# Optimization experiments

Hardware: AMD Instinct MI355X
Metric: run time of the kernel (lower is better)

Reference implementation:

```python
import jax, jax.numpy as jnp
import numpy as np

M, K, N, G = 4096, 4096, 4096, 128


def setup_inputs() -> dict:
    key = jax.random.key(0)
    k1, k2, k3 = jax.random.split(key, 3)
    a = jax.random.normal(k1, (M, K), dtype=jnp.float16)
    # 4-bit unsigned quantized weights, values in [0, 16)
    w_q = jax.random.randint(k2, (K, N), 0, 16, dtype=jnp.int32)
    # group-wise scales: one per (k-group, n); small magnitude keeps fp16 output in range
    scale = jax.random.uniform(k3, (K // G, N), dtype=jnp.float16, minval=0.001, maxval=0.02)
    return {"a": a, "w_q": w_q, "scale": scale, "group_size": G}


def reference(a, w_q, scale, group_size):
    # Dequantize: w[k, n] = w_q[k, n] * scale[k // group_size, n]
    scale_full = jnp.repeat(scale, group_size, axis=0)  # [K, N]
    w = w_q.astype(a.dtype) * scale_full                # fp16 dequantized weight
    out = jnp.matmul(a, w, preferred_element_type=jnp.float32)
    return out.astype(jnp.float16)
```

## Files before the change

### kernel.cpp

```cpp
#include <hip/hip_runtime.h>
#include <hip/hip_fp16.h>

#define MDIM 4096
#define NDIM 4096
#define KDIM 4096

#define BM 128
#define BN 128
#define BK 64
#define NT 256

typedef _Float16 f16x8 __attribute__((ext_vector_type(8)));
typedef float f32x4 __attribute__((ext_vector_type(4)));
typedef unsigned int u32;
typedef unsigned short u16;

__device__ inline __half2 as_half2(u32 u) { return __builtin_bit_cast(__half2, u); }
__device__ inline u32 as_u32(__half2 h) { return __builtin_bit_cast(u32, h); }
__device__ inline u32 pkrtz(float a, float b) {
  return __builtin_bit_cast(u32, __builtin_amdgcn_cvt_pkrtz(a, b));
}

__device__ inline void load16_to_lds(const void* g, void* l) {
  __builtin_amdgcn_global_load_lds(
      (__attribute__((address_space(1))) const u32*)g,
      (__attribute__((address_space(3))) u32*)l,
      16, 0, 0);
}

#define TSTR 68
#define WBLK 4096
__global__ __launch_bounds__(NT) void prep(const float* __restrict__ A,
                                           _Float16* __restrict__ A16,
                                           const int* __restrict__ Wq,
                                           const float* __restrict__ Sc,
                                           _Float16* __restrict__ Wt) {
  __shared__ __align__(16) u16 Ls[64 * TSTR];
  const int tid = threadIdx.x;

  if (blockIdx.x >= WBLK) {
    const size_t b = blockIdx.x - WBLK;
    const size_t base = (b * NT + tid) * 8;
    const float4 f0 = *(const float4*)(A + base);
    const float4 f1 = *(const float4*)(A + base + 4);
    u32 pk[4];
    pk[0] = pkrtz(f0.x, f0.y);
    pk[1] = pkrtz(f0.z, f0.w);
    pk[2] = pkrtz(f1.x, f1.y);
    pk[3] = pkrtz(f1.z, f1.w);
    *(uint4*)(A16 + base) = *(const uint4*)pk;
    return;
  }

  const int n0 = (blockIdx.x & 63) * 64;
  const int k0 = (blockIdx.x >> 6) * 64;
  const int g = k0 >> 7;

#pragma unroll
  for (int r = 0; r < 4; ++r) {
    const int c = r * 256 + tid;
    const int krow = c >> 4;
    const int col4 = (c & 15) * 4;
    const int4 v = *(const int4*)(Wq + (size_t)(k0 + krow) * NDIM + n0 + col4);
    const float4 s = *(const float4*)(Sc + (size_t)g * NDIM + n0 + col4);
    __half2 s01 = __floats2half2_rn(s.x, s.y);
    __half2 s23 = __floats2half2_rn(s.z, s.w);
    const __half2 kneg = __half2half2(__float2half(-1024.0f));
    __half2 nb01 = __hmul2(s01, kneg), nb23 = __hmul2(s23, kneg);
    u32 u01 = (u32)v.x | ((u32)v.y << 16) | 0x64006400u;
    u32 u23 = (u32)v.z | ((u32)v.w << 16) | 0x64006400u;
    u32 pk[2];
    pk[0] = as_u32(__hfma2(as_half2(u01), s01, nb01));
    pk[1] = as_u32(__hfma2(as_half2(u23), s23, nb23));
    *(uint2*)&Ls[(size_t)krow * TSTR + col4] = *(const uint2*)pk;
  }
  __syncthreads();

#pragma unroll
  for (int r = 0; r < 2; ++r) {
    const int idx = r * 256 + tid;
    const int n = idx >> 3;
    const int kc = (idx & 7) * 8;
    u16 tmp[8];
#pragma unroll
    for (int j = 0; j < 8; ++j) tmp[j] = Ls[(size_t)(kc + j) * TSTR + n];
    *(uint4*)(Wt + (size_t)(n0 + n) * KDIM + k0 + kc) = *(const uint4*)tmp;
  }
}

__global__ __launch_bounds__(NT) void gemm_f16(const _Float16* __restrict__ A16,
                                               const _Float16* __restrict__ Wt,
                                               float* __restrict__ C) {
  __shared__ __align__(16) _Float16 As[BM * BK];
  __shared__ __align__(16) _Float16 Bs[BN * BK];

  const int tid = threadIdx.x;
  const int bx = blockIdx.x & 31;
  const int by = blockIdx.x >> 5;
  const int m_base = by * BM;
  const int n_base = bx * BN;

  const int wave = tid >> 6;
  const int lane = tid & 63;
  const int l15 = lane & 15;
  const int quad = lane >> 4;
  const int wm = (wave & 1) * 64;
  const int wn = (wave >> 1) * 64;

  f32x4 acc[4][4];
#pragma unroll
  for (int i = 0; i < 4; ++i)
#pragma unroll
    for (int j = 0; j < 4; ++j) acc[i][j] = (f32x4)0.0f;

  for (int kt = 0; kt < KDIM / BK; ++kt) {
    const int k0 = kt * BK;
    __syncthreads();

#pragma unroll
    for (int r = 0; r < 4; ++r) {
      const int c = r * 256 + tid;
      const int row = c >> 3;
      const int gcol = (c & 7) ^ (row & 7);
      load16_to_lds(A16 + (size_t)(m_base + row) * KDIM + k0 + gcol * 8,
                    (char*)As + (size_t)c * 16);
      load16_to_lds(Wt + (size_t)(n_base + row) * KDIM + k0 + gcol * 8,
                    (char*)Bs + (size_t)c * 16);
    }
    __syncthreads();

#pragma unroll
    for (int ks = 0; ks < BK; ks += 32) {
      const int ksc = ks >> 3;
      f16x8 af[4], bf[4];
#pragma unroll
      for (int i = 0; i < 4; ++i) {
        const int row = wm + i * 16 + l15;
        af[i] = *(const f16x8*)&As[((size_t)row * 8 +
                                    ((ksc + quad) ^ (row & 7))) * 8];
      }
#pragma unroll
      for (int j = 0; j < 4; ++j) {
        const int row = wn + j * 16 + l15;
        bf[j] = *(const f16x8*)&Bs[((size_t)row * 8 +
                                    ((ksc + quad) ^ (row & 7))) * 8];
      }
#pragma unroll
      for (int i = 0; i < 4; ++i)
#pragma unroll
        for (int j = 0; j < 4; ++j)
          acc[i][j] = __builtin_amdgcn_mfma_f32_16x16x32_f16(af[i], bf[j],
                                                             acc[i][j], 0, 0, 0);
    }
  }

#pragma unroll
  for (int i = 0; i < 4; ++i) {
#pragma unroll
    for (int j = 0; j < 4; ++j) {
      const int col = n_base + wn + j * 16 + l15;
#pragma unroll
      for (int r = 0; r < 4; ++r) {
        const int row = m_base + wm + i * 16 + quad * 4 + r;
        C[(size_t)row * NDIM + col] = __half2float(__float2half(acc[i][j][r]));
      }
    }
  }
}

#define STR 72
__global__ __launch_bounds__(NT) void qgemm_fused(
    const float* __restrict__ A, const int* __restrict__ Wq,
    const float* __restrict__ Sc, float* __restrict__ C) {
  __shared__ __align__(16) _Float16 As[BM * STR];
  __shared__ __align__(16) _Float16 Bs[BN * STR];
  const int tid = threadIdx.x;
  const int bx = blockIdx.x & 31, by = blockIdx.x >> 5;
  const int m_base = by * BM, n_base = bx * BN;
  const int wave = tid >> 6, lane = tid & 63;
  const int l15 = lane & 15, quad = lane >> 4;
  const int wm = (wave & 1) * 64, wn = (wave >> 1) * 64;
  const int bn_local = tid & 127, bk_half = (tid >> 7) * 8;
  const int gn = n_base + bn_local;
  f32x4 acc[4][4];
#pragma unroll
  for (int i = 0; i < 4; ++i)
#pragma unroll
    for (int j = 0; j < 4; ++j) acc[i][j] = (f32x4)0.0f;
  for (int kt = 0; kt < KDIM / BK; ++kt) {
    const int k0 = kt * BK;
    __syncthreads();
#pragma unroll
    for (int i = 0; i < 8; ++i) {
      const int c = i * 256 + tid;
      const int row = c >> 4, col4 = (c & 15) * 4;
      const float4 f = *(const float4*)(A + (size_t)(m_base + row) * KDIM + k0 + col4);
      u32 pk[2];
      pk[0] = pkrtz(f.x, f.y);
      pk[1] = pkrtz(f.z, f.w);
      *(uint2*)&As[(size_t)row * STR + col4] = *(const uint2*)pk;
    }
    {
      const __half hs = __float2half(Sc[(size_t)(k0 >> 7) * NDIM + gn]);
      const __half2 s2 = __half2half2(hs);
      const __half2 nb2 = __half2half2(__hmul(hs, __float2half(-1024.0f)));
#pragma unroll
      for (int it = 0; it < 4; ++it) {
        const int k = bk_half + it * 16;
        u32 v[8];
#pragma unroll
        for (int j = 0; j < 8; ++j)
          v[j] = (u32)Wq[(size_t)(k0 + k + j) * NDIM + gn];
        u32 pk[4];
#pragma unroll
        for (int p = 0; p < 4; ++p) {
          u32 u = v[2 * p] | (v[2 * p + 1] << 16) | 0x64006400u;
          pk[p] = as_u32(__hfma2(as_half2(u), s2, nb2));
        }
        *(uint4*)&Bs[(size_t)bn_local * STR + k] = *(const uint4*)pk;
      }
    }
    __syncthreads();
#pragma unroll
    for (int ks = 0; ks < BK; ks += 32) {
      f16x8 af[4], bf[4];
#pragma unroll
      for (int i = 0; i < 4; ++i)
        af[i] = *(const f16x8*)&As[(size_t)(wm + i * 16 + l15) * STR + ks + quad * 8];
#pragma unroll
      for (int j = 0; j < 4; ++j)
        bf[j] = *(const f16x8*)&Bs[(size_t)(wn + j * 16 + l15) * STR + ks + quad * 8];
#pragma unroll
      for (int i = 0; i < 4; ++i)
#pragma unroll
        for (int j = 0; j < 4; ++j)
          acc[i][j] = __builtin_amdgcn_mfma_f32_16x16x32_f16(af[i], bf[j],
                                                             acc[i][j], 0, 0, 0);
    }
  }
#pragma unroll
  for (int i = 0; i < 4; ++i)
#pragma unroll
    for (int j = 0; j < 4; ++j) {
      const int col = n_base + wn + j * 16 + l15;
#pragma unroll
      for (int r = 0; r < 4; ++r) {
        const int row = m_base + wm + i * 16 + quad * 4 + r;
        C[(size_t)row * NDIM + col] = __half2float(__float2half(acc[i][j][r]));
      }
    }
}

extern "C" void kernel_launch(void* const* d_in, const int* in_sizes, int n_in,
                              void* d_out, int out_size, void* d_ws, size_t ws_size,
                              hipStream_t stream) {
  const float* a = (const float*)d_in[0];
  const int* wq = (const int*)d_in[1];
  const float* sc = (const float*)d_in[2];
  float* out = (float*)d_out;

  const size_t a16_bytes = (size_t)MDIM * KDIM * 2;
  const size_t wt_bytes = (size_t)NDIM * KDIM * 2;

  if (ws_size >= a16_bytes + wt_bytes) {
    _Float16* a16 = (_Float16*)d_ws;
    _Float16* wt = (_Float16*)((char*)d_ws + a16_bytes);
    const int a_blocks = (MDIM * KDIM) / (NT * 8);
    prep<<<WBLK + a_blocks, NT, 0, stream>>>(a, a16, wq, sc, wt);
    gemm_f16<<<(MDIM / BM) * (NDIM / BN), NT, 0, stream>>>(a16, wt, out);
  } else {
    qgemm_fused<<<(MDIM / BM) * (NDIM / BN), NT, 0, stream>>>(a, wq, sc, out);
  }
}
```

Baseline: 320.8 us.

## Use 256x256 tiles with a 4-stage async LDS pipeline in the fp16 GEMM

```diff
diff --git a/kernel.cpp b/kernel.cpp
--- a/kernel.cpp
+++ b/kernel.cpp
@@ -4,10 +4,6 @@
 #define MDIM 4096
 #define NDIM 4096
 #define KDIM 4096
-
-#define BM 128
-#define BN 128
-#define BK 64
 #define NT 256
 
 typedef _Float16 f16x8 __attribute__((ext_vector_type(8)));
@@ -28,30 +24,35 @@
       16, 0, 0);
 }
 
+template <int VM>
+__device__ __forceinline__ void wait_vmcnt() {
+  if constexpr (VM == 8)
+    asm volatile("s_waitcnt vmcnt(8)" ::: "memory");
+  else if constexpr (VM == 4)
+    asm volatile("s_waitcnt vmcnt(4)" ::: "memory");
+  else
+    asm volatile("s_waitcnt vmcnt(0)" ::: "memory");
+}
+
+__global__ __launch_bounds__(NT) void prep_a(const float* __restrict__ A,
+                                             _Float16* __restrict__ A16) {
+  const size_t base = ((size_t)blockIdx.x * NT + threadIdx.x) * 8;
+  const float4 f0 = *(const float4*)(A + base);
+  const float4 f1 = *(const float4*)(A + base + 4);
+  u32 pk[4];
+  pk[0] = pkrtz(f0.x, f0.y);
+  pk[1] = pkrtz(f0.z, f0.w);
+  pk[2] = pkrtz(f1.x, f1.y);
+  pk[3] = pkrtz(f1.z, f1.w);
+  *(uint4*)(A16 + base) = *(const uint4*)pk;
+}
+
 #define TSTR 68
-#define WBLK 4096
-__global__ __launch_bounds__(NT) void prep(const float* __restrict__ A,
-                                           _Float16* __restrict__ A16,
-                                           const int* __restrict__ Wq,
-                                           const float* __restrict__ Sc,
-                                           _Float16* __restrict__ Wt) {
+__global__ __launch_bounds__(NT) void prep_w(const int* __restrict__ Wq,
+                                             const float* __restrict__ Sc,
+                                             _Float16* __restrict__ Wt) {
   __shared__ __align__(16) u16 Ls[64 * TSTR];
   const int tid = threadIdx.x;
-
-  if (blockIdx.x >= WBLK) {
-    const size_t b = blockIdx.x - WBLK;
-    const size_t base = (b * NT + tid) * 8;
-    const float4 f0 = *(const float4*)(A + base);
-    const float4 f1 = *(const float4*)(A + base + 4);
-    u32 pk[4];
-    pk[0] = pkrtz(f0.x, f0.y);
-    pk[1] = pkrtz(f0.z, f0.w);
-    pk[2] = pkrtz(f1.x, f1.y);
-    pk[3] = pkrtz(f1.z, f1.w);
-    *(uint4*)(A16 + base) = *(const uint4*)pk;
-    return;
-  }
-
   const int n0 = (blockIdx.x & 63) * 64;
   const int k0 = (blockIdx.x >> 6) * 64;
   const int g = k0 >> 7;
@@ -88,80 +89,109 @@
   }
 }
 
-__global__ __launch_bounds__(NT) void gemm_f16(const _Float16* __restrict__ A16,
-                                               const _Float16* __restrict__ Wt,
-                                               float* __restrict__ C) {
-  __shared__ __align__(16) _Float16 As[BM * BK];
-  __shared__ __align__(16) _Float16 Bs[BN * BK];
+__global__ __launch_bounds__(512, 2) void gemm_f16(const _Float16* __restrict__ A16,
+                                                   const _Float16* __restrict__ Wt,
+                                                   float* __restrict__ C) {
+  __shared__ __align__(16) _Float16 As[4 * 256 * 32];
+  __shared__ __align__(16) _Float16 Bs[4 * 256 * 32];
 
   const int tid = threadIdx.x;
-  const int bx = blockIdx.x & 31;
-  const int by = blockIdx.x >> 5;
-  const int m_base = by * BM;
-  const int n_base = bx * BN;
+  const int bx = blockIdx.x & 15;
+  const int by = blockIdx.x >> 4;
+  const int m_base = by * 256;
+  const int n_base = bx * 256;
 
   const int wave = tid >> 6;
   const int lane = tid & 63;
   const int l15 = lane & 15;
   const int quad = lane >> 4;
-  const int wm = (wave & 1) * 64;
-  const int wn = (wave >> 1) * 64;
-
-  f32x4 acc[4][4];
-#pragma unroll
-  for (int i = 0; i < 4; ++i)
+  const int mq = wave >> 2;
+  const int nq = wave & 3;
+  const int gq = (l15 >> 1) & 3;
+  const int pchunk = quad ^ gq;
+
+  f32x4 acc[8][4];
+#pragma unroll
+  for (int i = 0; i < 8; ++i)
 #pragma unroll
     for (int j = 0; j < 4; ++j) acc[i][j] = (f32x4)0.0f;
 
-  for (int kt = 0; kt < KDIM / BK; ++kt) {
-    const int k0 = kt * BK;
-    __syncthreads();
-
-#pragma unroll
-    for (int r = 0; r < 4; ++r) {
-      const int c = r * 256 + tid;
-      const int row = c >> 3;
-      const int gcol = (c & 7) ^ (row & 7);
-      load16_to_lds(A16 + (size_t)(m_base + row) * KDIM + k0 + gcol * 8,
-                    (char*)As + (size_t)c * 16);
-      load16_to_lds(Wt + (size_t)(n_base + row) * KDIM + k0 + gcol * 8,
-                    (char*)Bs + (size_t)c * 16);
-    }
-    __syncthreads();
-
-#pragma unroll
-    for (int ks = 0; ks < BK; ks += 32) {
-      const int ksc = ks >> 3;
-      f16x8 af[4], bf[4];
-#pragma unroll
-      for (int i = 0; i < 4; ++i) {
-        const int row = wm + i * 16 + l15;
-        af[i] = *(const f16x8*)&As[((size_t)row * 8 +
-                                    ((ksc + quad) ^ (row & 7))) * 8];
-      }
-#pragma unroll
-      for (int j = 0; j < 4; ++j) {
-        const int row = wn + j * 16 + l15;
-        bf[j] = *(const f16x8*)&Bs[((size_t)row * 8 +
-                                    ((ksc + quad) ^ (row & 7))) * 8];
-      }
-#pragma unroll
-      for (int i = 0; i < 4; ++i)
-#pragma unroll
-        for (int j = 0; j < 4; ++j)
-          acc[i][j] = __builtin_amdgcn_mfma_f32_16x16x32_f16(af[i], bf[j],
-                                                             acc[i][j], 0, 0, 0);
-    }
-  }
-
-#pragma unroll
-  for (int i = 0; i < 4; ++i) {
+  auto stage = [&](int p) {
+    const int T = p >> 1;
+    const int h = p & 1;
+    const int s = p & 3;
+    const size_t kof = (size_t)T * 64 + (size_t)h * 32;
+#pragma unroll
+    for (int L = 0; L < 2; ++L) {
+      const int cc = L * 512 + tid;
+      const int row = cc >> 2;
+      const int lch = (cc & 3) ^ ((row >> 1) & 3);
+      load16_to_lds(A16 + (size_t)(m_base + row) * KDIM + kof + lch * 8,
+                    (char*)As + (size_t)s * 16384 + (size_t)cc * 16);
+    }
+#pragma unroll
+    for (int L = 0; L < 2; ++L) {
+      const int cc = L * 512 + tid;
+      const int row = cc >> 2;
+      const int lch = (cc & 3) ^ ((row >> 1) & 3);
+      load16_to_lds(Wt + (size_t)(n_base + row) * KDIM + kof + lch * 8,
+                    (char*)Bs + (size_t)s * 16384 + (size_t)cc * 16);
+    }
+  };
+
+  auto phase_body = [&](int p, bool dostage) {
+    __builtin_amdgcn_s_barrier();
+    asm volatile("" ::: "memory");
+    const int s = p & 3;
+    const _Float16* Ab = (const _Float16*)((const char*)As + (size_t)s * 16384);
+    const _Float16* Bb = (const _Float16*)((const char*)Bs + (size_t)s * 16384);
+    f16x8 af[8], bf[4];
+#pragma unroll
+    for (int i = 0; i < 8; ++i) {
+      const int row = mq * 128 + i * 16 + l15;
+      af[i] = *(const f16x8*)(Ab + (size_t)row * 32 + pchunk * 8);
+    }
 #pragma unroll
     for (int j = 0; j < 4; ++j) {
-      const int col = n_base + wn + j * 16 + l15;
+      const int row = nq * 64 + j * 16 + l15;
+      bf[j] = *(const f16x8*)(Bb + (size_t)row * 32 + pchunk * 8);
+    }
+    if (dostage) stage(p + 3);
+    asm volatile("s_waitcnt lgkmcnt(0)" ::: "memory");
+    __builtin_amdgcn_sched_barrier(0);
+    __builtin_amdgcn_s_setprio(1);
+#pragma unroll
+    for (int i = 0; i < 8; ++i)
+#pragma unroll
+      for (int j = 0; j < 4; ++j)
+        acc[i][j] = __builtin_amdgcn_mfma_f32_16x16x32_f16(af[i], bf[j],
+                                                           acc[i][j], 0, 0, 0);
+    __builtin_amdgcn_s_setprio(0);
+  };
+
+  stage(0);
+  stage(1);
+  stage(2);
+
+  for (int p = 0; p < 125; ++p) {
+    wait_vmcnt<8>();
+    phase_body(p, true);
+  }
+  wait_vmcnt<8>();
+  phase_body(125, false);
+  wait_vmcnt<4>();
+  phase_body(126, false);
+  wait_vmcnt<0>();
+  phase_body(127, false);
+
+#pragma unroll
+  for (int i = 0; i < 8; ++i) {
+#pragma unroll
+    for (int j = 0; j < 4; ++j) {
+      const int col = n_base + nq * 64 + j * 16 + l15;
 #pragma unroll
       for (int r = 0; r < 4; ++r) {
-        const int row = m_base + wm + i * 16 + quad * 4 + r;
+        const int row = m_base + mq * 128 + i * 16 + quad * 4 + r;
         C[(size_t)row * NDIM + col] = __half2float(__float2half(acc[i][j][r]));
       }
     }
@@ -172,11 +202,11 @@
 __global__ __launch_bounds__(NT) void qgemm_fused(
     const float* __restrict__ A, const int* __restrict__ Wq,
     const float* __restrict__ Sc, float* __restrict__ C) {
-  __shared__ __align__(16) _Float16 As[BM * STR];
-  __shared__ __align__(16) _Float16 Bs[BN * STR];
+  __shared__ __align__(16) _Float16 As[128 * STR];
+  __shared__ __align__(16) _Float16 Bs[128 * STR];
   const int tid = threadIdx.x;
   const int bx = blockIdx.x & 31, by = blockIdx.x >> 5;
-  const int m_base = by * BM, n_base = bx * BN;
+  const int m_base = by * 128, n_base = bx * 128;
   const int wave = tid >> 6, lane = tid & 63;
   const int l15 = lane & 15, quad = lane >> 4;
   const int wm = (wave & 1) * 64, wn = (wave >> 1) * 64;
@@ -187,8 +217,8 @@
   for (int i = 0; i < 4; ++i)
 #pragma unroll
     for (int j = 0; j < 4; ++j) acc[i][j] = (f32x4)0.0f;
-  for (int kt = 0; kt < KDIM / BK; ++kt) {
-    const int k0 = kt * BK;
+  for (int kt = 0; kt < KDIM / 64; ++kt) {
+    const int k0 = kt * 64;
     __syncthreads();
 #pragma unroll
     for (int i = 0; i < 8; ++i) {
@@ -222,7 +252,7 @@
     }
     __syncthreads();
 #pragma unroll
-    for (int ks = 0; ks < BK; ks += 32) {
+    for (int ks = 0; ks < 64; ks += 32) {
       f16x8 af[4], bf[4];
 #pragma unroll
       for (int i = 0; i < 4; ++i)
@@ -265,10 +295,10 @@
   if (ws_size >= a16_bytes + wt_bytes) {
     _Float16* a16 = (_Float16*)d_ws;
     _Float16* wt = (_Float16*)((char*)d_ws + a16_bytes);
-    const int a_blocks = (MDIM * KDIM) / (NT * 8);
-    prep<<<WBLK + a_blocks, NT, 0, stream>>>(a, a16, wq, sc, wt);
-    gemm_f16<<<(MDIM / BM) * (NDIM / BN), NT, 0, stream>>>(a16, wt, out);
+    prep_a<<<(MDIM * KDIM) / (NT * 8), NT, 0, stream>>>(a, a16);
+    prep_w<<<(KDIM / 64) * (NDIM / 64), NT, 0, stream>>>(wq, sc, wt);
+    gemm_f16<<<(MDIM / 256) * (NDIM / 256), 512, 0, stream>>>(a16, wt, out);
   } else {
-    qgemm_fused<<<(MDIM / BM) * (NDIM / BN), NT, 0, stream>>>(a, wq, sc, out);
-  }
-}
+    qgemm_fused<<<(MDIM / 128) * (NDIM / 128), NT, 0, stream>>>(a, wq, sc, out);
+  }
+}
```

After: 291.0 us. 9.3% less time.
